# Performance work log

Measured on AMD Instinct MI355X. Metric: run time of the kernel, lower is better.

## Reference

```python
import jax, jax.numpy as jnp
import numpy as np

H = 64

def _gru(x, Wih, Whh, bih, bhh):
    # x: [NB, L, D]; torch GRU gate order: r, z, n
    h0 = jnp.zeros((x.shape[0], Whh.shape[1]), x.dtype)
    def step(h, xt):
        gi = xt @ Wih.T + bih
        gh = h @ Whh.T + bhh
        ir, iz, inn = jnp.split(gi, 3, axis=-1)
        hr, hz, hn = jnp.split(gh, 3, axis=-1)
        r = jax.nn.sigmoid(ir + hr)
        z = jax.nn.sigmoid(iz + hz)
        n = jnp.tanh(inn + r * hn)
        h_new = (1.0 - z) * n + z * h
        return h_new, h_new
    hT, ys = jax.lax.scan(step, h0, jnp.swapaxes(x, 0, 1))
    return jnp.swapaxes(ys, 0, 1), hT  # outputs [NB,L,H], last hidden [NB,H]


def setup_inputs() -> dict:
    key = jax.random.key(0)
    ks = jax.random.split(key, 20)
    N, B, L, D = 2000, 8, 12, 2
    E = 16000
    s = 0.1
    return {
        "data": jax.random.normal(ks[0], (N, B, L, D), jnp.float32),
        "features": jax.random.normal(ks[1], (N, H), jnp.float32),
        "edge_index": jax.random.randint(ks[2], (2, E), 0, N, jnp.int64 if jax.config.jax_enable_x64 else jnp.int32),
        "Wih1": jax.random.normal(ks[3], (3 * H, D), jnp.float32) * s,
        "Whh1": jax.random.normal(ks[4], (3 * H, H), jnp.float32) * s,
        "bih1": jax.random.normal(ks[5], (3 * H,), jnp.float32) * s,
        "bhh1": jax.random.normal(ks[6], (3 * H,), jnp.float32) * s,
        "W1": jax.random.normal(ks[7], (16, 2 * H), jnp.float32) * s,
        "b1": jax.random.normal(ks[8], (16,), jnp.float32) * s,
        "W2": jax.random.normal(ks[9], (2, 16), jnp.float32) * s,
        "b2": jax.random.normal(ks[10], (2,), jnp.float32) * s,
        "W3": jax.random.normal(ks[11], (2 * H * H, 2), jnp.float32) * s,
        "b3": jax.random.normal(ks[12], (2 * H * H,), jnp.float32) * s,
        "Wih2": jax.random.normal(ks[13], (3 * H, H), jnp.float32) * s,
        "Whh2": jax.random.normal(ks[14], (3 * H, H), jnp.float32) * s,
        "bih2": jax.random.normal(ks[15], (3 * H,), jnp.float32) * s,
        "bhh2": jax.random.normal(ks[16], (3 * H,), jnp.float32) * s,
    }


def reference(data, features, edge_index, Wih1, Whh1, bih1, bhh1,
              W1, b1, W2, b2, W3, b3, Wih2, Whh2, bih2, bhh2):
    N, B, L, D = data.shape
    # --- first GRU over [N*B, L, D] ---
    out1, h1 = _gru(data.reshape(N * B, L, D), Wih1, Whh1, bih1, bhh1)
    out1 = out1.reshape(N, B, L, H)
    h1 = h1.reshape(N, B, H)
    # --- MetaGAT with self loops ---
    loops = jnp.arange(N, dtype=edge_index.dtype)
    src = jnp.concatenate([edge_index[0], loops])  # j (source)
    dst = jnp.concatenate([edge_index[1], loops])  # i (target)
    states_j = out1[src]                 # [E', B, L, H]
    states_i = out1[dst]
    feats = jnp.concatenate([features[dst], features[src]], axis=-1)  # [E', 2H]
    # per-edge MLP generating weights
    hdn = jax.nn.sigmoid(feats @ W1.T + b1)
    hdn = jax.nn.sigmoid(hdn @ W2.T + b2)
    w = (hdn @ W3.T + b3).reshape(-1, 2 * H, H)  # [E', 2H, H]
    states = jnp.concatenate([states_i, states_j], axis=-1)  # [E', B, L, 2H]
    alpha = jax.nn.leaky_relu(jnp.einsum('eblk,ekh->eblh', states, w))
    alpha = jax.nn.softmax(alpha, axis=1)  # softmax over batch dim, as in source
    msg = alpha * states_j                 # [E', B, L, H]
    agg = jax.ops.segment_sum(msg, dst, num_segments=N)
    out2 = jax.nn.relu(agg)                # [N, B, L, H]
    # --- second GRU ---
    _, h2 = _gru(out2.reshape(N * B, L, H), Wih2, Whh2, bih2, bhh2)
    h2 = h2.reshape(N, B, H)
    return h1, h2
```

## Files before the change

kernel.cpp:

```cpp
#include <hip/hip_runtime.h>
#include <hip/hip_bf16.h>

typedef unsigned short ushort_t;
typedef unsigned int uint_t;
typedef __attribute__((ext_vector_type(8))) short bf16x8;
typedef __attribute__((ext_vector_type(4))) float f32x4;

#define NNODE 2000
#define NB 8
#define LSEQ 12
#define HDIM 64
#define NEDGE 16000
#define NSEQ (NNODE * NB)
#define OUT1_ELEMS (NNODE * NB * LSEQ * HDIM)
#define OUT1_BYTES (OUT1_ELEMS * 2)
#define AGG_BYTES  (OUT1_ELEMS * 2)
#define SST 72
#define LOG2E 1.4426950408889634f

#define WFRAG_ELEMS (6 * 2 * 256 * 8)
#define G2FRAG_ELEMS (3 * 2 * 2 * 256 * 8)

__device__ __forceinline__ float bf1(ushort_t u) { return __uint_as_float(((uint_t)u) << 16); }
__device__ __forceinline__ ushort_t fbf(float f) {
    uint_t x = __float_as_uint(f);
    uint_t r = x + 0x7fffu + ((x >> 16) & 1u);
    return (ushort_t)(r >> 16);
}
__device__ __forceinline__ float sigm(float x) {
    return __builtin_amdgcn_rcpf(1.f + __expf(-x));
}
__device__ __forceinline__ float tanh_fast(float x) {
    return 2.f * __builtin_amdgcn_rcpf(1.f + __expf(-2.f * x)) - 1.f;
}


__global__ __launch_bounds__(256) void mega_kernel(
    const float* __restrict__ data, const float* __restrict__ Wih,
    const float* __restrict__ Whh, const float* __restrict__ bih,
    const float* __restrict__ bhh, ushort_t* __restrict__ out1,
    float* __restrict__ h1out,
    const int* __restrict__ edges, int* __restrict__ degree,
    int* __restrict__ rowstart, int* __restrict__ srcids,
    int* __restrict__ eids, int* __restrict__ order,
    const float* __restrict__ features,
    const float* __restrict__ W1, const float* __restrict__ b1,
    const float* __restrict__ W2, const float* __restrict__ b2,
    float* __restrict__ alphas,
    const float* __restrict__ W3, const float* __restrict__ b3,
    const float* __restrict__ Wih2, const float* __restrict__ Whh2,
    ushort_t* __restrict__ wfrag, ushort_t* __restrict__ g2frag)
{
    __shared__ ushort_t H[2][16][SST] __attribute__((aligned(16)));
    __shared__ float XD[16][26];
    __shared__ int hist[NNODE];
    __shared__ int wsum[4];
    __shared__ float m1[4][16];
    __shared__ int dh[64];

    const int bx = blockIdx.x;
    const int tid = threadIdx.x;

    if (bx == 5501) {
        {
            const int wv = tid >> 6, r = tid & 15, quad = (tid >> 4) & 3;
            const int n = wv * 16 + r;
#pragma unroll
            for (int ks = 0; ks < 2; ++ks) {
                ushort_t ta[8], tb[8], tc[8], ba[8], bb[8], bc[8];
#pragma unroll
                for (int jj = 0; jj < 8; ++jj) {
                    const int mt_ = (ks * 32 + quad * 8 + jj) * 64 + n;
                    float2 w2 = ((const float2*)W3)[mt_];
                    ta[jj] = fbf(w2.x * LOG2E); tb[jj] = fbf(w2.y * LOG2E);
                    tc[jj] = fbf(b3[mt_] * LOG2E);
                    const int mb_ = (64 + ks * 32 + quad * 8 + jj) * 64 + n;
                    float2 w2b = ((const float2*)W3)[mb_];
                    ba[jj] = fbf(w2b.x * LOG2E); bb[jj] = fbf(w2b.y * LOG2E);
                    bc[jj] = fbf(b3[mb_] * LOG2E);
                }
                *(uint4*)(wfrag + ((0 * 2 + ks) * 256 + tid) * 8) = *(uint4*)ta;
                *(uint4*)(wfrag + ((1 * 2 + ks) * 256 + tid) * 8) = *(uint4*)tb;
                *(uint4*)(wfrag + ((2 * 2 + ks) * 256 + tid) * 8) = *(uint4*)tc;
                *(uint4*)(wfrag + ((3 * 2 + ks) * 256 + tid) * 8) = *(uint4*)ba;
                *(uint4*)(wfrag + ((4 * 2 + ks) * 256 + tid) * 8) = *(uint4*)bb;
                *(uint4*)(wfrag + ((5 * 2 + ks) * 256 + tid) * 8) = *(uint4*)bc;
            }
        }
        {
            const int nw = tid >> 6, c = tid & 15, quad = (tid >> 4) & 3;
            const int j = nw * 16 + c;
#pragma unroll
            for (int g = 0; g < 3; ++g) {
                const int row = g * 64 + j;
#pragma unroll
                for (int ks = 0; ks < 2; ++ks) {
                    const float* wp = Whh2 + (row << 6) + ks * 32 + quad * 8;
                    float4 wa = *(const float4*)wp;
                    float4 wb = *(const float4*)(wp + 4);
                    ushort_t tmp[8];
                    tmp[0] = fbf(wa.x); tmp[1] = fbf(wa.y); tmp[2] = fbf(wa.z); tmp[3] = fbf(wa.w);
                    tmp[4] = fbf(wb.x); tmp[5] = fbf(wb.y); tmp[6] = fbf(wb.z); tmp[7] = fbf(wb.w);
                    *(uint4*)(g2frag + (((g * 2 + ks) * 2 + 0) * 256 + tid) * 8) = *(uint4*)tmp;
                    const float* wp2 = Wih2 + (row << 6) + ks * 32 + quad * 8;
                    float4 va = *(const float4*)wp2;
                    float4 vb = *(const float4*)(wp2 + 4);
                    tmp[0] = fbf(va.x); tmp[1] = fbf(va.y); tmp[2] = fbf(va.z); tmp[3] = fbf(va.w);
                    tmp[4] = fbf(vb.x); tmp[5] = fbf(vb.y); tmp[6] = fbf(vb.z); tmp[7] = fbf(vb.w);
                    *(uint4*)(g2frag + (((g * 2 + ks) * 2 + 1) * 256 + tid) * 8) = *(uint4*)tmp;
                }
            }
        }
        return;
    }

    if (bx == 1000) {
        for (int k = tid; k < NNODE; k += 256) hist[k] = 0;
        if (tid < 64) dh[tid] = 0;
        __syncthreads();
        for (int it = 0; it < 16; ++it) {
            const int e0 = it * 1024 + tid * 4;
            if (e0 + 3 < NEDGE) {
                int4 v4 = *(const int4*)(edges + NEDGE + e0);
                atomicAdd(&hist[v4.x], 1);
                atomicAdd(&hist[v4.y], 1);
                atomicAdd(&hist[v4.z], 1);
                atomicAdd(&hist[v4.w], 1);
            } else {
#pragma unroll
                for (int k = 0; k < 4; ++k) {
                    const int e = e0 + k;
                    if (e < NEDGE) atomicAdd(&hist[edges[NEDGE + e]], 1);
                }
            }
        }
        __syncthreads();
        const int lane = tid & 63, w = tid >> 6;
        int d[8];
        int s = 0;
#pragma unroll
        for (int q = 0; q < 8; ++q) {
            const int idx = tid * 8 + q;
            d[q] = (idx < NNODE) ? hist[idx] : 0;
            s += d[q];
        }
        int v = s;
#pragma unroll
        for (int off = 1; off < 64; off <<= 1) {
            int u = __shfl_up(v, off);
            if (lane >= off) v += u;
        }
        if (lane == 63) wsum[w] = v;
        __syncthreads();
        int base = 0;
        for (int k = 0; k < 4; ++k) if (k < w) base += wsum[k];
        int run = base + v - s;
        int rs8[8];
#pragma unroll
        for (int q = 0; q < 8; ++q) {
            const int idx = tid * 8 + q;
            if (idx < NNODE) {
                rs8[q] = run;
                rowstart[idx] = run;
                degree[idx] = d[q];
                run += d[q];
                atomicAdd(&dh[63 - min(d[q], 63)], 1);
            }
        }
        __syncthreads();
        if (tid == 0) {
            int acc = 0;
            for (int k = 0; k < 64; ++k) { const int c = dh[k]; dh[k] = acc; acc += c; }
        }
        __syncthreads();
#pragma unroll
        for (int q = 0; q < 8; ++q) {
            const int idx = tid * 8 + q;
            if (idx < NNODE) {
                const int pos = atomicAdd(&dh[63 - min(d[q], 63)], 1);
                order[pos] = idx;
            }
        }
        __syncthreads();
#pragma unroll
        for (int q = 0; q < 8; ++q) {
            const int idx = tid * 8 + q;
            if (idx < NNODE) hist[idx] = rs8[q];
        }
        __syncthreads();
        for (int it = 0; it < 16; ++it) {
            const int e0 = it * 1024 + tid * 4;
            if (e0 + 3 < NEDGE) {
                int4 dv4 = *(const int4*)(edges + NEDGE + e0);
                int4 sv4 = *(const int4*)(edges + e0);
                int pos;
                pos = atomicAdd(&hist[dv4.x], 1); srcids[pos] = sv4.x; eids[pos] = e0;
                pos = atomicAdd(&hist[dv4.y], 1); srcids[pos] = sv4.y; eids[pos] = e0 + 1;
                pos = atomicAdd(&hist[dv4.z], 1); srcids[pos] = sv4.z; eids[pos] = e0 + 2;
                pos = atomicAdd(&hist[dv4.w], 1); srcids[pos] = sv4.w; eids[pos] = e0 + 3;
            } else {
#pragma unroll
                for (int k = 0; k < 4; ++k) {
                    const int e = e0 + k;
                    if (e < NEDGE) {
                        const int pos = atomicAdd(&hist[edges[NEDGE + e]], 1);
                        srcids[pos] = edges[e];
                        eids[pos] = e;
                    }
                }
            }
        }
        return;
    }

    if (bx > 1000) {
        const int w = tid >> 6, lane = tid & 63;
        const int e = (bx - 1001) * 4 + w;
        int i, j;
        if (e < NEDGE) { j = edges[e]; i = edges[NEDGE + e]; }
        else { i = j = e - NEDGE; }
        const int o = lane >> 2, q = lane & 3;
        const float* fsrc = (q < 2) ? (features + i * 64 + q * 32)
                                    : (features + j * 64 + (q - 2) * 32);
        const float* wsrc = W1 + o * 128 + q * 32;
        float acc = 0.f;
#pragma unroll
        for (int k = 0; k < 32; ++k) acc += fsrc[k] * wsrc[k];
        acc += __shfl_xor(acc, 1);
        acc += __shfl_xor(acc, 2);
        if (q == 0) m1[w][o] = sigm(acc + b1[o]);
        __syncthreads();
        if (lane < 32 && e < NEDGE + NNODE) {
            const int o2 = lane >> 4, k = lane & 15;
            float p = m1[w][k] * W2[o2 * 16 + k];
            p += __shfl_xor(p, 1);
            p += __shfl_xor(p, 2);
            p += __shfl_xor(p, 4);
            p += __shfl_xor(p, 8);
            if (k == 0) alphas[e * 2 + o2] = sigm(p + b2[o2]);
        }
        return;
    }

    const int nw = tid >> 6;
    const int c = tid & 15;
    const int quad = (tid >> 4) & 3;
    const int j = nw * 16 + c;
    const int s0 = bx * 16;
    const int crow = tid >> 4, ccol = (tid & 15) * 4;

    if (tid < 128) *(uint4*)&H[0][tid >> 3][(tid & 7) * 8] = uint4{0, 0, 0, 0};
#pragma unroll
    for (int p = 0; p < 2; ++p) {
        const int flat = p * 256 + tid;
        if (flat < 384) {
            const int sl = flat / 24, q = flat - sl * 24;
            XD[sl][q] = data[(s0 + sl) * 24 + q];
        }
    }

    bf16x8 Bh[3][2];
    float wi0[3], wi1[3], bi[3], bh[3];
#pragma unroll
    for (int g = 0; g < 3; ++g) {
        const int row = g * 64 + j;
        float2 wi = *(const float2*)(Wih + row * 2);
        wi0[g] = wi.x; wi1[g] = wi.y;
        bi[g] = bih[row]; bh[g] = bhh[row];
#pragma unroll
        for (int ks = 0; ks < 2; ++ks) {
            const float* wp = Whh + (row << 6) + ks * 32 + quad * 8;
            float4 wa = *(const float4*)wp;
            float4 wb = *(const float4*)(wp + 4);
            ushort_t tmp[8];
            tmp[0] = fbf(wa.x); tmp[1] = fbf(wa.y); tmp[2] = fbf(wa.z); tmp[3] = fbf(wa.w);
            tmp[4] = fbf(wb.x); tmp[5] = fbf(wb.y); tmp[6] = fbf(wb.z); tmp[7] = fbf(wb.w);
            Bh[g][ks] = *(bf16x8*)tmp;
        }
    }

    float hold[4];
#pragma unroll
    for (int rg = 0; rg < 4; ++rg) hold[rg] = 0.f;

    for (int t = 0; t < LSEQ; ++t) {
        __syncthreads();
        const ushort_t (*Hr)[SST] = H[t & 1];
        ushort_t (*Hw)[SST] = H[1 - (t & 1)];
        bf16x8 a0 = *(const bf16x8*)&Hr[c][quad * 8];
        bf16x8 a1 = *(const bf16x8*)&Hr[c][32 + quad * 8];
        if (t > 0)
            *(uint2*)(out1 + (s0 + crow) * (LSEQ * HDIM) + (t - 1) * HDIM + ccol) =
                *(const uint2*)&Hr[crow][ccol];
        f32x4 gh[3];
#pragma unroll
        for (int g = 0; g < 3; ++g) {
            f32x4 acc = {0.f, 0.f, 0.f, 0.f};
            acc = __builtin_amdgcn_mfma_f32_16x16x32_bf16(a0, Bh[g][0], acc, 0, 0, 0);
            acc = __builtin_amdgcn_mfma_f32_16x16x32_bf16(a1, Bh[g][1], acc, 0, 0, 0);
            gh[g] = acc;
        }
#pragma unroll
        for (int rg = 0; rg < 4; ++rg) {
            const int sloc = quad * 4 + rg;
            float2 xp = *(const float2*)&XD[sloc][2 * t];
            float gr = bh[0] + gh[0][rg];
            float gz = bh[1] + gh[1][rg];
            float gn = bh[2] + gh[2][rg];
            float ir = bi[0] + wi0[0] * xp.x + wi1[0] * xp.y;
            float iz = bi[1] + wi0[1] * xp.x + wi1[1] * xp.y;
            float in = bi[2] + wi0[2] * xp.x + wi1[2] * xp.y;
            float r = sigm(ir + gr);
            float z = sigm(iz + gz);
            float n = tanh_fast(in + r * gn);
            float hv = (1.f - z) * n + z * hold[rg];
            hold[rg] = hv;
            Hw[sloc][j] = fbf(hv);
        }
    }
    __syncthreads();
    *(uint2*)(out1 + (s0 + crow) * (LSEQ * HDIM) + (LSEQ - 1) * HDIM + ccol) =
        *(const uint2*)&H[LSEQ & 1][crow][ccol];
#pragma unroll
    for (int rg = 0; rg < 4; ++rg) {
        const int sloc = quad * 4 + rg;
        h1out[(s0 + sloc) * HDIM + j] = hold[rg];
    }
}

__global__ __launch_bounds__(256) void gat_csr_kernel(
    const ushort_t* __restrict__ out1,
    const int* __restrict__ degree, const int* __restrict__ rowstart,
    const int* __restrict__ srcids, const int* __restrict__ eids,
    const int* __restrict__ order,
    const float* __restrict__ alphas,
    const ushort_t* __restrict__ wfrag,
    ushort_t* __restrict__ agg)
{
    __shared__ ushort_t POOL[4][32][SST] __attribute__((aligned(16)));

    const int tid = threadIdx.x;
    const int i = order[blockIdx.x];
    const int mh = blockIdx.y;
    const int deg = degree[i];
    const int rs = rowstart[i];

    const int wv = tid >> 6;
    const int r = tid & 15;
    const int quad = (tid >> 4) & 3;
    const int n = wv * 16 + r;

    const float2 aSelf = *(const float2*)(alphas + (NEDGE + i) * 2);

    int glo[2], lso[2];
#pragma unroll
    for (int p = 0; p < 2; ++p) {
        const int u = p * 256 + tid;
        const int rr = u >> 4, c4 = u & 15;
        const int b = rr & 7, l = (rr >> 3) + 4 * mh;
        glo[p] = (b * 12 + l) * 64 + c4 * 4;
        lso[p] = rr * SST + c4 * 4;
    }
    int afo[2][2];
#pragma unroll
    for (int mt = 0; mt < 2; ++mt) {
        afo[mt][0] = (mt * 16 + r) * SST + quad * 8;
        afo[mt][1] = afo[mt][0] + 32;
    }
    int cbo[2];
#pragma unroll
    for (int mt = 0; mt < 2; ++mt)
        cbo[mt] = (mt * 16 + quad * 4) * SST + (n & ~1);
    const uint_t shamt = (n & 1) ? 0u : 16u;

    const ushort_t* pi = out1 + i * (NB * LSEQ * HDIM);
    ushort_t* const sbase = &POOL[0][0][0];
    ushort_t* const Si = sbase;

#pragma unroll
    for (int p = 0; p < 2; ++p)
        *(uint2*)(Si + lso[p]) = *(const uint2*)(pi + glo[p]);

    bf16x8 WtA[2], WtB[2], WtC[2], WbA[2], WbB[2], WbC[2];
#pragma unroll
    for (int ks = 0; ks < 2; ++ks) {
        WtA[ks] = *(const bf16x8*)(wfrag + ((0 * 2 + ks) * 256 + tid) * 8);
        WtB[ks] = *(const bf16x8*)(wfrag + ((1 * 2 + ks) * 256 + tid) * 8);
        WtC[ks] = *(const bf16x8*)(wfrag + ((2 * 2 + ks) * 256 + tid) * 8);
        WbA[ks] = *(const bf16x8*)(wfrag + ((3 * 2 + ks) * 256 + tid) * 8);
        WbB[ks] = *(const bf16x8*)(wfrag + ((4 * 2 + ks) * 256 + tid) * 8);
        WbC[ks] = *(const bf16x8*)(wfrag + ((5 * 2 + ks) * 256 + tid) * 8);
    }

    __syncthreads();

    f32x4 PA[2], PB[2], PC[2];
#pragma unroll
    for (int mt = 0; mt < 2; ++mt) {
        bf16x8 af0 = *(const bf16x8*)(Si + afo[mt][0]);
        bf16x8 af1 = *(const bf16x8*)(Si + afo[mt][1]);
        f32x4 pa = {0.f, 0.f, 0.f, 0.f};
        f32x4 pb = {0.f, 0.f, 0.f, 0.f};
        f32x4 pc = {0.f, 0.f, 0.f, 0.f};
        pa = __builtin_amdgcn_mfma_f32_16x16x32_bf16(af0, WtA[0], pa, 0, 0, 0);
        pa = __builtin_amdgcn_mfma_f32_16x16x32_bf16(af1, WtA[1], pa, 0, 0, 0);
        pb = __builtin_amdgcn_mfma_f32_16x16x32_bf16(af0, WtB[0], pb, 0, 0, 0);
        pb = __builtin_amdgcn_mfma_f32_16x16x32_bf16(af1, WtB[1], pb, 0, 0, 0);
        pc = __builtin_amdgcn_mfma_f32_16x16x32_bf16(af0, WtC[0], pc, 0, 0, 0);
        pc = __builtin_amdgcn_mfma_f32_16x16x32_bf16(af1, WtC[1], pc, 0, 0, 0);
        PA[mt] = pa; PB[mt] = pb; PC[mt] = pc;
    }

    float accN[2][4];
#pragma unroll
    for (int mt = 0; mt < 2; ++mt)
#pragma unroll
        for (int g2 = 0; g2 < 4; ++g2) accN[mt][g2] = 0.f;

    auto process = [&](const ushort_t* SB, float2 a01) {
#pragma unroll
        for (int mt = 0; mt < 2; ++mt) {
            bf16x8 aj0 = *(const bf16x8*)(SB + afo[mt][0]);
            bf16x8 aj1 = *(const bf16x8*)(SB + afo[mt][1]);
            const uint_t* dp = (const uint_t*)(SB + cbo[mt]);
            uint_t d0 = dp[0], d1 = dp[36], d2 = dp[72], d3 = dp[108];
            f32x4 aA = PA[mt], aB = PB[mt], aC = PC[mt];
            aA = __builtin_amdgcn_mfma_f32_16x16x32_bf16(aj0, WbA[0], aA, 0, 0, 0);
            aA = __builtin_amdgcn_mfma_f32_16x16x32_bf16(aj1, WbA[1], aA, 0, 0, 0);
            aB = __builtin_amdgcn_mfma_f32_16x16x32_bf16(aj0, WbB[0], aB, 0, 0, 0);
            aB = __builtin_amdgcn_mfma_f32_16x16x32_bf16(aj1, WbB[1], aB, 0, 0, 0);
            aC = __builtin_amdgcn_mfma_f32_16x16x32_bf16(aj0, WbC[0], aC, 0, 0, 0);
            aC = __builtin_amdgcn_mfma_f32_16x16x32_bf16(aj1, WbC[1], aC, 0, 0, 0);
            float v[4];
            float s = 0.f;
#pragma unroll
            for (int g2 = 0; g2 < 4; ++g2) {
                float x = fmaf(a01.x, aA[g2], fmaf(a01.y, aB[g2], aC[g2]));
                x = fmaxf(x, 0.01f * x);
                v[g2] = __builtin_amdgcn_exp2f(x);
                s += v[g2];
            }
            s += __shfl_xor(s, 16);
            const float inv = __builtin_amdgcn_rcpf(s);
            uint_t dd[4] = {d0, d1, d2, d3};
#pragma unroll
            for (int g2 = 0; g2 < 4; ++g2) {
                const float sj = __uint_as_float((dd[g2] << shamt) & 0xFFFF0000u);
                accN[mt][g2] += v[g2] * inv * sj;
            }
        }
    };

    int sa_nxt = 0, sb_nxt = 0, eA1 = 0, eB1 = 0;
    float2 aA_cur = float2{0.f, 0.f}, aB_cur = float2{0.f, 0.f};
    if (deg >= 1) { const int e = eids[rs];     aA_cur = *(const float2*)(alphas + e * 2); }
    if (deg >= 2) { const int e = eids[rs + 1]; aB_cur = *(const float2*)(alphas + e * 2); }
    if (deg >= 3) { sa_nxt = srcids[rs + 2]; eA1 = eids[rs + 2]; }
    if (deg >= 4) { sb_nxt = srcids[rs + 3]; eB1 = eids[rs + 3]; }

    uint2 pfA[2], pfB[2];
    {
        const ushort_t* pA = out1 + ((deg >= 1) ? srcids[rs] : 0) * (NB * LSEQ * HDIM);
        const ushort_t* pB = out1 + ((deg >= 2) ? srcids[rs + 1] : 0) * (NB * LSEQ * HDIM);
#pragma unroll
        for (int p = 0; p < 2; ++p) {
            pfA[p] = *(const uint2*)(pA + glo[p]);
            pfB[p] = *(const uint2*)(pB + glo[p]);
        }
    }

    process(Si, aSelf);
    __syncthreads();

    const int npairs = (deg + 1) >> 1;
    for (int pk = 0; pk < npairs; ++pk) {
        ushort_t* SA = sbase + (2 * (pk & 1)) * (32 * SST);
        ushort_t* SB = SA + 32 * SST;
#pragma unroll
        for (int p = 0; p < 2; ++p) {
            *(uint2*)(SA + lso[p]) = pfA[p];
            *(uint2*)(SB + lso[p]) = pfB[p];
        }
        const int base = pk * 2;
        const bool hasB = (base + 1) < deg;

        int sa_n2 = 0, sb_n2 = 0, eA2 = 0, eB2 = 0;
        if (base + 4 < deg) { sa_n2 = srcids[rs + base + 4]; eA2 = eids[rs + base + 4]; }
        if (base + 5 < deg) { sb_n2 = srcids[rs + base + 5]; eB2 = eids[rs + base + 5]; }
        float2 aA_n = float2{0.f, 0.f}, aB_n = float2{0.f, 0.f};
        if (base + 2 < deg) aA_n = *(const float2*)(alphas + eA1 * 2);
        if (base + 3 < deg) aB_n = *(const float2*)(alphas + eB1 * 2);

        __syncthreads();

        if (base + 2 < deg) {
            const ushort_t* pA = out1 + sa_nxt * (NB * LSEQ * HDIM);
#pragma unroll
            for (int p = 0; p < 2; ++p) pfA[p] = *(const uint2*)(pA + glo[p]);
        }
        if (base + 3 < deg) {
            const ushort_t* pB = out1 + sb_nxt * (NB * LSEQ * HDIM);
#pragma unroll
            for (int p = 0; p < 2; ++p) pfB[p] = *(const uint2*)(pB + glo[p]);
        }

        process(SA, aA_cur);
        if (hasB) process(SB, aB_cur);

        aA_cur = aA_n; aB_cur = aB_n;
        sa_nxt = sa_n2; sb_nxt = sb_n2;
        eA1 = eA2; eB1 = eB2;
    }

#pragma unroll
    for (int mt = 0; mt < 2; ++mt)
#pragma unroll
        for (int g2 = 0; g2 < 4; ++g2) {
            const int gr = mh * 32 + mt * 16 + quad * 4 + g2;
            const int b = gr & 7, l = gr >> 3;
            agg[(i * 96 + b * 12 + l) * 64 + n] = fbf(accN[mt][g2]);
        }
}

__global__ __launch_bounds__(256) void gru2_kernel(
    const ushort_t* __restrict__ agg, const ushort_t* __restrict__ g2frag,
    const float* __restrict__ bih, const float* __restrict__ bhh,
    float* __restrict__ h2out)
{
    __shared__ ushort_t H[2][16][SST] __attribute__((aligned(16)));
    __shared__ ushort_t X[2][16][SST] __attribute__((aligned(16)));

    const int tid = threadIdx.x;
    const int nw = tid >> 6;
    const int c = tid & 15;
    const int quad = (tid >> 4) & 3;
    const int j = nw * 16 + c;
    const int s0 = blockIdx.x * 16;
    const int sl = tid >> 3, k0 = (tid & 7) * 8;

    if (tid < 128) *(uint4*)&H[0][tid >> 3][(tid & 7) * 8] = uint4{0, 0, 0, 0};

    bf16x8 Bh[3][2], Bi[3][2];
    float bi[3], bh[3];
#pragma unroll
    for (int g = 0; g < 3; ++g) {
        const int row = g * 64 + j;
        bi[g] = bih[row]; bh[g] = bhh[row];
#pragma unroll
        for (int ks = 0; ks < 2; ++ks) {
            Bh[g][ks] = *(const bf16x8*)(g2frag + (((g * 2 + ks) * 2 + 0) * 256 + tid) * 8);
            Bi[g][ks] = *(const bf16x8*)(g2frag + (((g * 2 + ks) * 2 + 1) * 256 + tid) * 8);
        }
    }

    float hold[4];
#pragma unroll
    for (int rg = 0; rg < 4; ++rg) hold[rg] = 0.f;

    if (tid < 128) {
        ushort_t xr[8];
        *(uint4*)xr = *(const uint4*)(agg + (s0 + sl) * (LSEQ * HDIM) + k0);
        ushort_t xs[8];
#pragma unroll
        for (int q = 0; q < 8; ++q) xs[q] = (xr[q] & 0x8000u) ? (ushort_t)0 : xr[q];
        *(uint4*)&X[0][sl][k0] = *(uint4*)xs;
    }

    for (int t = 0; t < LSEQ; ++t) {
        __syncthreads();
        const int rb = t & 1, wb = 1 - rb;
        bf16x8 ah0 = *(const bf16x8*)&H[rb][c][quad * 8];
        bf16x8 ah1 = *(const bf16x8*)&H[rb][c][32 + quad * 8];
        bf16x8 ax0 = *(const bf16x8*)&X[rb][c][quad * 8];
        bf16x8 ax1 = *(const bf16x8*)&X[rb][c][32 + quad * 8];

        ushort_t xr[8];
        if (t < LSEQ - 1 && tid < 128)
            *(uint4*)xr = *(const uint4*)(agg + (s0 + sl) * (LSEQ * HDIM) +
                                          (t + 1) * HDIM + k0);

        f32x4 gh[3], gi[3];
#pragma unroll
        for (int g = 0; g < 3; ++g) {
            f32x4 acc = {0.f, 0.f, 0.f, 0.f};
            acc = __builtin_amdgcn_mfma_f32_16x16x32_bf16(ah0, Bh[g][0], acc, 0, 0, 0);
            acc = __builtin_amdgcn_mfma_f32_16x16x32_bf16(ah1, Bh[g][1], acc, 0, 0, 0);
            gh[g] = acc;
            f32x4 acc2 = {0.f, 0.f, 0.f, 0.f};
            acc2 = __builtin_amdgcn_mfma_f32_16x16x32_bf16(ax0, Bi[g][0], acc2, 0, 0, 0);
            acc2 = __builtin_amdgcn_mfma_f32_16x16x32_bf16(ax1, Bi[g][1], acc2, 0, 0, 0);
            gi[g] = acc2;
        }
#pragma unroll
        for (int rg = 0; rg < 4; ++rg) {
            const int sloc = quad * 4 + rg;
            float r = sigm(bi[0] + gi[0][rg] + bh[0] + gh[0][rg]);
            float z = sigm(bi[1] + gi[1][rg] + bh[1] + gh[1][rg]);
            float n = tanh_fast(bi[2] + gi[2][rg] + r * (bh[2] + gh[2][rg]));
            float hv = (1.f - z) * n + z * hold[rg];
            hold[rg] = hv;
            H[wb][sloc][j] = fbf(hv);
        }
        if (t < LSEQ - 1 && tid < 128) {
            ushort_t xs[8];
#pragma unroll
            for (int q = 0; q < 8; ++q) xs[q] = (xr[q] & 0x8000u) ? (ushort_t)0 : xr[q];
            *(uint4*)&X[wb][sl][k0] = *(uint4*)xs;
        }
    }
#pragma unroll
    for (int rg = 0; rg < 4; ++rg) {
        const int sloc = quad * 4 + rg;
        h2out[(s0 + sloc) * HDIM + j] = hold[rg];
    }
}

extern "C" void kernel_launch(void* const* d_in, const int* in_sizes, int n_in,
                              void* d_out, int out_size, void* d_ws, size_t ws_size,
                              hipStream_t stream)
{
    const float* data     = (const float*)d_in[0];
    const float* features = (const float*)d_in[1];
    const int*   edges    = (const int*)d_in[2];
    const float* Wih1     = (const float*)d_in[3];
    const float* Whh1     = (const float*)d_in[4];
    const float* bih1     = (const float*)d_in[5];
    const float* bhh1     = (const float*)d_in[6];
    const float* W1       = (const float*)d_in[7];
    const float* b1       = (const float*)d_in[8];
    const float* W2       = (const float*)d_in[9];
    const float* b2       = (const float*)d_in[10];
    const float* W3       = (const float*)d_in[11];
    const float* b3       = (const float*)d_in[12];
    const float* Wih2     = (const float*)d_in[13];
    const float* Whh2     = (const float*)d_in[14];
    const float* bih2     = (const float*)d_in[15];
    const float* bhh2     = (const float*)d_in[16];

    float*    out  = (float*)d_out;
    char*     ws   = (char*)d_ws;
    ushort_t* out1 = (ushort_t*)ws;
    ushort_t* agg  = (ushort_t*)(ws + OUT1_BYTES);
    int*      meta = (int*)(ws + OUT1_BYTES + AGG_BYTES);
    int*   degree   = meta;
    int*   rowstart = meta + NNODE;
    int*   srcids   = meta + 2 * NNODE;
    int*   eids     = meta + 2 * NNODE + NEDGE;
    int*   order    = meta + 2 * NNODE + 2 * NEDGE;
    float* alphas   = (float*)(meta + 3 * NNODE + 2 * NEDGE);
    ushort_t* wfrag  = (ushort_t*)((char*)alphas + 36000 * 4);
    ushort_t* g2frag = wfrag + WFRAG_ELEMS;

    mega_kernel<<<1001 + 4500 + 1, 256, 0, stream>>>(
        data, Wih1, Whh1, bih1, bhh1, out1, out,
        edges, degree, rowstart, srcids, eids, order,
        features, W1, b1, W2, b2, alphas,
        W3, b3, Wih2, Whh2, wfrag, g2frag);
    gat_csr_kernel<<<dim3(NNODE, 3), 256, 0, stream>>>(out1, degree, rowstart, srcids,
                                                       eids, order, alphas, wfrag, agg);
    gru2_kernel<<<NSEQ / 16, 256, 0, stream>>>(agg, g2frag, bih2, bhh2,
                                               out + NNODE * NB * HDIM);
}
```

Baseline: 226.0 us.

## Reorder mega-kernel blocks, record CSR ranks, stage GRU I/O through LDS

Moves the CSR-build and weight-prep blocks to the start of the grid so they are scheduled first instead of trailing behind the GRU blocks. The histogram pass now records each edge's rank, so the scatter pass needs no second round of atomics. GRU1 outputs are buffered in a shared-memory tile and written with coalesced 16-byte stores at the end instead of per-step stores. GRU2 preloads its whole input sequence into LDS up front, and the edge MLP uses float4 loads. Shared memory is now a single aliased buffer, which raises LDS use per block and may lower occupancy.

```diff
diff --git a/kernel.cpp b/kernel.cpp
--- a/kernel.cpp
+++ b/kernel.cpp
@@ -43,6 +43,7 @@
     const int* __restrict__ edges, int* __restrict__ degree,
     int* __restrict__ rowstart, int* __restrict__ srcids,
     int* __restrict__ eids, int* __restrict__ order,
+    int* __restrict__ rank_,
     const float* __restrict__ features,
     const float* __restrict__ W1, const float* __restrict__ b1,
     const float* __restrict__ W2, const float* __restrict__ b2,
@@ -51,17 +52,19 @@
     const float* __restrict__ Wih2, const float* __restrict__ Whh2,
     ushort_t* __restrict__ wfrag, ushort_t* __restrict__ g2frag)
 {
-    __shared__ ushort_t H[2][16][SST] __attribute__((aligned(16)));
-    __shared__ float XD[16][26];
-    __shared__ int hist[NNODE];
-    __shared__ int wsum[4];
-    __shared__ float m1[4][16];
-    __shared__ int dh[64];
+    __shared__ __attribute__((aligned(16))) char SMEM[30848];
+    ushort_t (*H)[16][SST]  = (ushort_t (*)[16][SST])SMEM;
+    float    (*XD)[26]      = (float (*)[26])(SMEM + 4608);
+    ushort_t (*HT)[12][64]  = (ushort_t (*)[12][64])(SMEM + 6272);
+    int* hist = (int*)SMEM;
+    int* dh   = (int*)(SMEM + 8000);
+    int* wsum = (int*)(SMEM + 8256);
+    float (*m1)[16] = (float (*)[16])SMEM;
 
     const int bx = blockIdx.x;
     const int tid = threadIdx.x;
 
-    if (bx == 5501) {
+    if (bx == 1) {
         {
             const int wv = tid >> 6, r = tid & 15, quad = (tid >> 4) & 3;
             const int n = wv * 16 + r;
@@ -114,7 +117,7 @@
         return;
     }
 
-    if (bx == 1000) {
+    if (bx == 0) {
         for (int k = tid; k < NNODE; k += 256) hist[k] = 0;
         if (tid < 64) dh[tid] = 0;
         __syncthreads();
@@ -122,15 +125,17 @@
             const int e0 = it * 1024 + tid * 4;
             if (e0 + 3 < NEDGE) {
                 int4 v4 = *(const int4*)(edges + NEDGE + e0);
-                atomicAdd(&hist[v4.x], 1);
-                atomicAdd(&hist[v4.y], 1);
-                atomicAdd(&hist[v4.z], 1);
-                atomicAdd(&hist[v4.w], 1);
+                int4 rk;
+                rk.x = atomicAdd(&hist[v4.x], 1);
+                rk.y = atomicAdd(&hist[v4.y], 1);
+                rk.z = atomicAdd(&hist[v4.z], 1);
+                rk.w = atomicAdd(&hist[v4.w], 1);
+                *(int4*)(rank_ + e0) = rk;
             } else {
 #pragma unroll
                 for (int k = 0; k < 4; ++k) {
                     const int e = e0 + k;
-                    if (e < NEDGE) atomicAdd(&hist[edges[NEDGE + e]], 1);
+                    if (e < NEDGE) rank_[e] = atomicAdd(&hist[edges[NEDGE + e]], 1);
                 }
             }
         }
@@ -193,17 +198,18 @@
             if (e0 + 3 < NEDGE) {
                 int4 dv4 = *(const int4*)(edges + NEDGE + e0);
                 int4 sv4 = *(const int4*)(edges + e0);
+                int4 rk4 = *(const int4*)(rank_ + e0);
                 int pos;
-                pos = atomicAdd(&hist[dv4.x], 1); srcids[pos] = sv4.x; eids[pos] = e0;
-                pos = atomicAdd(&hist[dv4.y], 1); srcids[pos] = sv4.y; eids[pos] = e0 + 1;
-                pos = atomicAdd(&hist[dv4.z], 1); srcids[pos] = sv4.z; eids[pos] = e0 + 2;
-                pos = atomicAdd(&hist[dv4.w], 1); srcids[pos] = sv4.w; eids[pos] = e0 + 3;
+                pos = hist[dv4.x] + rk4.x; srcids[pos] = sv4.x; eids[pos] = e0;
+                pos = hist[dv4.y] + rk4.y; srcids[pos] = sv4.y; eids[pos] = e0 + 1;
+                pos = hist[dv4.z] + rk4.z; srcids[pos] = sv4.z; eids[pos] = e0 + 2;
+                pos = hist[dv4.w] + rk4.w; srcids[pos] = sv4.w; eids[pos] = e0 + 3;
             } else {
 #pragma unroll
                 for (int k = 0; k < 4; ++k) {
                     const int e = e0 + k;
                     if (e < NEDGE) {
-                        const int pos = atomicAdd(&hist[edges[NEDGE + e]], 1);
+                        const int pos = hist[edges[NEDGE + e]] + rank_[e];
                         srcids[pos] = edges[e];
                         eids[pos] = e;
                     }
@@ -213,9 +219,9 @@
         return;
     }
 
-    if (bx > 1000) {
+    if (bx > 1001) {
         const int w = tid >> 6, lane = tid & 63;
-        const int e = (bx - 1001) * 4 + w;
+        const int e = (bx - 1002) * 4 + w;
         int i, j;
         if (e < NEDGE) { j = edges[e]; i = edges[NEDGE + e]; }
         else { i = j = e - NEDGE; }
@@ -223,9 +229,17 @@
         const float* fsrc = (q < 2) ? (features + i * 64 + q * 32)
                                     : (features + j * 64 + (q - 2) * 32);
         const float* wsrc = W1 + o * 128 + q * 32;
+        const float4* f4 = (const float4*)fsrc;
+        const float4* w4 = (const float4*)wsrc;
         float acc = 0.f;
 #pragma unroll
-        for (int k = 0; k < 32; ++k) acc += fsrc[k] * wsrc[k];
+        for (int k = 0; k < 8; ++k) {
+            float4 a = f4[k], b = w4[k];
+            acc = fmaf(a.x, b.x, acc);
+            acc = fmaf(a.y, b.y, acc);
+            acc = fmaf(a.z, b.z, acc);
+            acc = fmaf(a.w, b.w, acc);
+        }
         acc += __shfl_xor(acc, 1);
         acc += __shfl_xor(acc, 2);
         if (q == 0) m1[w][o] = sigm(acc + b1[o]);
@@ -246,8 +260,7 @@
     const int c = tid & 15;
     const int quad = (tid >> 4) & 3;
     const int j = nw * 16 + c;
-    const int s0 = bx * 16;
-    const int crow = tid >> 4, ccol = (tid & 15) * 4;
+    const int s0 = (bx - 2) * 16;
 
     if (tid < 128) *(uint4*)&H[0][tid >> 3][(tid & 7) * 8] = uint4{0, 0, 0, 0};
 #pragma unroll
@@ -289,9 +302,6 @@
         ushort_t (*Hw)[SST] = H[1 - (t & 1)];
         bf16x8 a0 = *(const bf16x8*)&Hr[c][quad * 8];
         bf16x8 a1 = *(const bf16x8*)&Hr[c][32 + quad * 8];
-        if (t > 0)
-            *(uint2*)(out1 + (s0 + crow) * (LSEQ * HDIM) + (t - 1) * HDIM + ccol) =
-                *(const uint2*)&Hr[crow][ccol];
         f32x4 gh[3];
 #pragma unroll
         for (int g = 0; g < 3; ++g) {
@@ -315,12 +325,20 @@
             float n = tanh_fast(in + r * gn);
             float hv = (1.f - z) * n + z * hold[rg];
             hold[rg] = hv;
-            Hw[sloc][j] = fbf(hv);
+            const ushort_t hv16 = fbf(hv);
+            Hw[sloc][j] = hv16;
+            HT[sloc][t][j] = hv16;
         }
     }
     __syncthreads();
-    *(uint2*)(out1 + (s0 + crow) * (LSEQ * HDIM) + (LSEQ - 1) * HDIM + ccol) =
-        *(const uint2*)&H[LSEQ & 1][crow][ccol];
+    {
+        const ushort_t* HTf = &HT[0][0][0];
+#pragma unroll
+        for (int q = 0; q < 6; ++q) {
+            const int idx8 = (q * 256 + tid) * 8;
+            *(uint4*)(out1 + s0 * (LSEQ * HDIM) + idx8) = *(const uint4*)(HTf + idx8);
+        }
+    }
 #pragma unroll
     for (int rg = 0; rg < 4; ++rg) {
         const int sloc = quad * 4 + rg;
@@ -528,7 +546,7 @@
     float* __restrict__ h2out)
 {
     __shared__ ushort_t H[2][16][SST] __attribute__((aligned(16)));
-    __shared__ ushort_t X[2][16][SST] __attribute__((aligned(16)));
+    __shared__ ushort_t XA[16][LSEQ][SST] __attribute__((aligned(16)));
 
     const int tid = threadIdx.x;
     const int nw = tid >> 6;
@@ -536,9 +554,25 @@
     const int quad = (tid >> 4) & 3;
     const int j = nw * 16 + c;
     const int s0 = blockIdx.x * 16;
-    const int sl = tid >> 3, k0 = (tid & 7) * 8;
 
     if (tid < 128) *(uint4*)&H[0][tid >> 3][(tid & 7) * 8] = uint4{0, 0, 0, 0};
+
+    {
+        const ushort_t* src = agg + s0 * (LSEQ * HDIM);
+#pragma unroll
+        for (int q = 0; q < 6; ++q) {
+            const int idx8 = (q * 256 + tid) * 8;
+            ushort_t xr[8];
+            *(uint4*)xr = *(const uint4*)(src + idx8);
+            ushort_t xs[8];
+#pragma unroll
+            for (int qq = 0; qq < 8; ++qq) xs[qq] = (xr[qq] & 0x8000u) ? (ushort_t)0 : xr[qq];
+            const int seq = idx8 / (LSEQ * HDIM);
+            const int rem = idx8 - seq * (LSEQ * HDIM);
+            const int t = rem >> 6, k = rem & 63;
+            *(uint4*)&XA[seq][t][k] = *(uint4*)xs;
+        }
+    }
 
     bf16x8 Bh[3][2], Bi[3][2];
     float bi[3], bh[3];
@@ -557,27 +591,13 @@
 #pragma unroll
     for (int rg = 0; rg < 4; ++rg) hold[rg] = 0.f;
 
-    if (tid < 128) {
-        ushort_t xr[8];
-        *(uint4*)xr = *(const uint4*)(agg + (s0 + sl) * (LSEQ * HDIM) + k0);
-        ushort_t xs[8];
-#pragma unroll
-        for (int q = 0; q < 8; ++q) xs[q] = (xr[q] & 0x8000u) ? (ushort_t)0 : xr[q];
-        *(uint4*)&X[0][sl][k0] = *(uint4*)xs;
-    }
-
     for (int t = 0; t < LSEQ; ++t) {
         __syncthreads();
         const int rb = t & 1, wb = 1 - rb;
         bf16x8 ah0 = *(const bf16x8*)&H[rb][c][quad * 8];
         bf16x8 ah1 = *(const bf16x8*)&H[rb][c][32 + quad * 8];
-        bf16x8 ax0 = *(const bf16x8*)&X[rb][c][quad * 8];
-        bf16x8 ax1 = *(const bf16x8*)&X[rb][c][32 + quad * 8];
-
-        ushort_t xr[8];
-        if (t < LSEQ - 1 && tid < 128)
-            *(uint4*)xr = *(const uint4*)(agg + (s0 + sl) * (LSEQ * HDIM) +
-                                          (t + 1) * HDIM + k0);
+        bf16x8 ax0 = *(const bf16x8*)&XA[c][t][quad * 8];
+        bf16x8 ax1 = *(const bf16x8*)&XA[c][t][32 + quad * 8];
 
         f32x4 gh[3], gi[3];
 #pragma unroll
@@ -600,12 +620,6 @@
             float hv = (1.f - z) * n + z * hold[rg];
             hold[rg] = hv;
             H[wb][sloc][j] = fbf(hv);
-        }
-        if (t < LSEQ - 1 && tid < 128) {
-            ushort_t xs[8];
-#pragma unroll
-            for (int q = 0; q < 8; ++q) xs[q] = (xr[q] & 0x8000u) ? (ushort_t)0 : xr[q];
-            *(uint4*)&X[wb][sl][k0] = *(uint4*)xs;
         }
     }
 #pragma unroll
@@ -650,10 +664,11 @@
     float* alphas   = (float*)(meta + 3 * NNODE + 2 * NEDGE);
     ushort_t* wfrag  = (ushort_t*)((char*)alphas + 36000 * 4);
     ushort_t* g2frag = wfrag + WFRAG_ELEMS;
-
-    mega_kernel<<<1001 + 4500 + 1, 256, 0, stream>>>(
+    int*      rank_  = (int*)(g2frag + G2FRAG_ELEMS);
+
+    mega_kernel<<<5502, 256, 0, stream>>>(
         data, Wih1, Whh1, bih1, bhh1, out1, out,
-        edges, degree, rowstart, srcids, eids, order,
+        edges, degree, rowstart, srcids, eids, order, rank_,
         features, W1, b1, W2, b2, alphas,
         W3, b3, Wih2, Whh2, wfrag, g2frag);
     gat_csr_kernel<<<dim3(NNODE, 3), 256, 0, stream>>>(out1, degree, rowstart, srcids,
```

Result: slower. 232.8 us (+3.0%).
